# Performance work log

Measured on AMD Instinct MI355X. Metric: run time of the kernel, lower is better.

The kernel has to match this reference:

```python
import jax, jax.numpy as jnp
import numpy as np

B, S, D, H = 4, 2048, 1024, 16
DH = D // H


def setup_inputs() -> dict:
    key = jax.random.key(0)
    ks = jax.random.split(key, 6)
    scale = 1.0 / np.sqrt(D)  # xavier-ish scale for weights
    return {
        "x": jax.random.normal(ks[0], (B, S, D), dtype=jnp.float32),
        "M": jax.random.normal(ks[1], (B, D, D), dtype=jnp.float32) * scale,
        "mask": jnp.zeros((1, 1, S, S), dtype=jnp.float32),
        "Wq": jax.random.normal(ks[2], (D, D), dtype=jnp.float32) * scale,
        "Wk": jax.random.normal(ks[3], (D, D), dtype=jnp.float32) * scale,
        "Wv": jax.random.normal(ks[4], (D, D), dtype=jnp.float32) * scale,
        "Wo": jax.random.normal(ks[5], (D, D), dtype=jnp.float32) * scale,
    }


def reference(x, M, mask, Wq, Wk, Wv, Wo):
    # Projections (torch Linear: y = x @ W^T, bias=False)
    Q = jnp.einsum('bsd,ed->bse', x, Wq)
    K = jnp.einsum('bsd,ed->bse', x, Wk)
    V = jnp.einsum('bsd,ed->bse', x, Wv)
    # Archetypal metric: QM = Q @ M, per-batch bilinear transform on full d_model
    QM = jnp.einsum('bsd,bde->bse', Q, M)

    def split(t):  # [B,S,D] -> [B,H,S,DH]
        return t.reshape(B, S, H, DH).transpose(0, 2, 1, 3)

    QMh, Kh, Vh = split(QM), split(K), split(V)
    scores = jnp.einsum('bhsd,bhtd->bhst', QMh, Kh) / np.sqrt(DH)
    scores = jnp.clip(scores, -50.0, 50.0)
    scores = scores + mask  # broadcast additive mask
    attn = jax.nn.softmax(scores, axis=-1)  # dropout is identity (eval)
    out = jnp.einsum('bhst,bhtd->bhsd', attn, Vh)
    out = out.transpose(0, 2, 1, 3).reshape(B, S, D)  # merge heads
    return jnp.einsum('bsd,ed->bse', out, Wo)
```

## Files before the change

kernel.cpp:

```cpp
#include <hip/hip_runtime.h>
#include <cstdint>

typedef __attribute__((ext_vector_type(8))) short short8;
typedef __attribute__((ext_vector_type(8))) __bf16 bf16x8;
typedef __attribute__((ext_vector_type(4))) float f32x4;

__device__ __forceinline__ uint32_t cvt_pk_bf16(float lo, float hi) {
  uint32_t r;
  asm("v_cvt_pk_bf16_f32 %0, %1, %2" : "=v"(r) : "v"(lo), "v"(hi));
  return r;
}

__device__ __forceinline__ short f2bf(float f) {
  return (short)cvt_pk_bf16(f, f);
}

__device__ __forceinline__ float exp2_fast(float x) {
  return __builtin_amdgcn_exp2f(x);
}

__device__ __forceinline__ void mem_fence_compiler() {
  asm volatile("" ::: "memory");
}

__device__ __forceinline__ void gload_lds16(const void* g, void* l) {
  __builtin_amdgcn_global_load_lds(
      (const __attribute__((address_space(1))) void*)(uintptr_t)g,
      (__attribute__((address_space(3))) void*)(uint32_t)(uintptr_t)l,
      16, 0, 0);
}


__global__ __launch_bounds__(256) void cvt_f32_bf16(const float* __restrict__ s,
                                                    short* __restrict__ d, long n) {
  long i = ((long)blockIdx.x * 256 + threadIdx.x) * 8;
  if (i + 8 > n) return;
  const float4 a = *(const float4*)(s + i);
  const float4 b = *(const float4*)(s + i + 4);
  uint4 o;
  o.x = cvt_pk_bf16(a.x, a.y);
  o.y = cvt_pk_bf16(a.z, a.w);
  o.z = cvt_pk_bf16(b.x, b.y);
  o.w = cvt_pk_bf16(b.z, b.w);
  *(uint4*)(d + i) = o;
}

__global__ __launch_bounds__(256) void cvtT_M(const float* __restrict__ Msrc,
                                              short* __restrict__ Mt) {
  __shared__ short t[64][65];
  const int tid = threadIdx.x;
  const long bofs = (long)blockIdx.z * 1024 * 1024;
  const int d0 = blockIdx.x * 64, e0 = blockIdx.y * 64;
#pragma unroll
  for (int k = 0; k < 16; ++k) {
    int idx = k * 256 + tid; int r = idx >> 6, c = idx & 63;
    t[r][c] = f2bf(Msrc[bofs + (long)(d0 + r) * 1024 + e0 + c]);
  }
  __syncthreads();
#pragma unroll
  for (int k = 0; k < 16; ++k) {
    int idx = k * 256 + tid; int r = idx >> 6, c = idx & 63;
    Mt[bofs + (long)(e0 + r) * 1024 + d0 + c] = t[c][r];
  }
}

__global__ __launch_bounds__(256) void transposeV(const short* __restrict__ V,
                                                  short* __restrict__ Vt) {
  __shared__ short t[64][65];
  const int tid = threadIdx.x;
  const int s0 = blockIdx.x * 64, h = blockIdx.y;
  const long b = blockIdx.z;
  const short* src = V + (b * 2048) * 1024 + h * 64;
  short* dst = Vt + ((b * 16 + h) * 64) * 2048;
#pragma unroll
  for (int k = 0; k < 16; ++k) {
    int idx = k * 256 + tid; int r = idx >> 6, c = idx & 63;
    t[r][c] = src[(long)(s0 + r) * 1024 + c];
  }
  __syncthreads();
#pragma unroll
  for (int k = 0; k < 16; ++k) {
    int idx = k * 256 + tid; int r = idx >> 6, c = idx & 63;
    dst[(long)r * 2048 + s0 + c] = t[c][r];
  }
}

__global__ __launch_bounds__(256) void mask_flags(const float* __restrict__ mask,
                                                  int* __restrict__ flags) {
  __shared__ int f;
  const int tid = threadIdx.x;
  if (tid == 0) f = 0;
  __syncthreads();
  const int qt = blockIdx.x, tt = blockIdx.y;
  const float* base = mask + (long)qt * 64 * 2048 + tt * 64;
  const int r = tid >> 2, c = (tid & 3) * 16;
  bool nz = false;
#pragma unroll
  for (int k = 0; k < 4; ++k) {
    float4 v = *(const float4*)(base + (long)r * 2048 + c + k * 4);
    nz = nz | (v.x != 0.f) | (v.y != 0.f) | (v.z != 0.f) | (v.w != 0.f);
  }
  if (nz) f = 1;
  __syncthreads();
  if (tid == 0) flags[qt * 32 + tt] = f;
}


template <typename CT>
__global__ __launch_bounds__(256) void gemm_bt(
    const short* __restrict__ A, const short* __restrict__ B, CT* __restrict__ C,
    int M, int N, int K, long sA, long sB, long sC, float scale) {
  __shared__ __align__(16) short As[2][128 * 32];
  __shared__ __align__(16) short Bs[2][128 * 32];
  const int tid = threadIdx.x;
  const int w = tid >> 6, lane = tid & 63;
  const int wr = w >> 1, wc = w & 1;
  const int g = lane >> 4;
  const short* Ab = A + (long)blockIdx.z * sA + (long)blockIdx.x * 128 * K;
  const short* Bb = B + (long)blockIdx.z * sB + (long)blockIdx.y * 128 * K;

  f32x4 acc[4][4];
#pragma unroll
  for (int i = 0; i < 4; ++i)
#pragma unroll
    for (int j = 0; j < 4; ++j) acc[i][j] = {0.f, 0.f, 0.f, 0.f};

  const int srow = lane >> 2;
  const int scol = ((lane & 3) ^ (srow & 3)) * 8;

  auto STAGE = [&](int bufi, int k0) {
#pragma unroll
    for (int c = 0; c < 2; ++c) {
      const int chunk = w * 2 + c;
      const long gr = (long)(chunk * 16 + srow);
      gload_lds16(Ab + gr * K + k0 + scol, &As[bufi][chunk * 512]);
      gload_lds16(Bb + gr * K + k0 + scol, &Bs[bufi][chunk * 512]);
    }
  };

  auto COMPUTE = [&](int bufi) {
    bf16x8 af[4], bfr[4];
#pragma unroll
    for (int mf = 0; mf < 4; ++mf) {
      const int r = wr * 64 + mf * 16 + (lane & 15);
      const int cb = g ^ (r & 3);
      af[mf] = *(const bf16x8*)&As[bufi][r * 32 + cb * 8];
    }
#pragma unroll
    for (int nf = 0; nf < 4; ++nf) {
      const int r = wc * 64 + nf * 16 + (lane & 15);
      const int cb = g ^ (r & 3);
      bfr[nf] = *(const bf16x8*)&Bs[bufi][r * 32 + cb * 8];
    }
#pragma unroll
    for (int mf = 0; mf < 4; ++mf)
#pragma unroll
      for (int nf = 0; nf < 4; ++nf)
        acc[mf][nf] =
            __builtin_amdgcn_mfma_f32_16x16x32_bf16(af[mf], bfr[nf], acc[mf][nf], 0, 0, 0);
  };

  const int NK = K >> 5;
  STAGE(0, 0);
  for (int it = 0; it < NK; ++it) {
    const int cur = it & 1;
    if (it + 1 < NK) {
      STAGE(cur ^ 1, (it + 1) * 32);
      asm volatile("s_waitcnt vmcnt(4)" ::: "memory");
    } else {
      asm volatile("s_waitcnt vmcnt(0)" ::: "memory");
    }
    __builtin_amdgcn_s_barrier();
    __builtin_amdgcn_sched_barrier(0);
    COMPUTE(cur);
    __builtin_amdgcn_sched_barrier(0);
    __builtin_amdgcn_s_barrier();
  }

  CT* Cb = C + (long)blockIdx.z * sC;
  const int r0 = g * 4, cc = lane & 15;
#pragma unroll
  for (int mf = 0; mf < 4; ++mf)
#pragma unroll
    for (int i = 0; i < 4; ++i) {
      const long row = (long)blockIdx.x * 128 + wr * 64 + mf * 16 + r0 + i;
#pragma unroll
      for (int nf = 0; nf < 4; ++nf) {
        const long col = (long)blockIdx.y * 128 + wc * 64 + nf * 16 + cc;
        float v = acc[mf][nf][i] * scale;
        if constexpr (__is_same(CT, short))
          Cb[row * (long)N + col] = f2bf(v);
        else
          Cb[row * (long)N + col] = v;
      }
    }
}


__global__ __launch_bounds__(512) void flash_attn(
    const short* __restrict__ QM, const short* __restrict__ Kb,
    const short* __restrict__ Vt, const float* __restrict__ mask,
    const int* __restrict__ mflags, short* __restrict__ AO) {
  constexpr int S = 2048, D = 1024, NT = S / 64;
  constexpr float LOG2E = 1.44269504088896f;
  constexpr float CLIP = 50.0f * LOG2E;
  __shared__ __align__(16) short Ks[2][64 * 64];
  __shared__ __align__(16) short Vs[2][64 * 64];
  __shared__ __align__(16) short Ps[8][16 * 64];
  const int tid = threadIdx.x;
  const int w = tid >> 6, lane = tid & 63;
  const int q = lane & 15, g = lane >> 4;
  const int q0 = blockIdx.x * 128;
  const int h = blockIdx.y;
  const long b = blockIdx.z;

  const short* QMb = QM + (b * S) * D + h * 64;
  const short* Kbp = Kb + (b * S) * D + h * 64;
  const short* Vtp = Vt + ((b * 16 + h) * 64) * S;
  const int* flagrow = mflags + ((q0 + w * 16) >> 6) * 32;

  bf16x8 qf[2];
#pragma unroll
  for (int ks = 0; ks < 2; ++ks)
    qf[ks] = *(const bf16x8*)(QMb + (long)(q0 + w * 16 + q) * D + ks * 32 + g * 8);

  bf16x8 onesf;
#pragma unroll
  for (int j = 0; j < 8; ++j) onesf[j] = (__bf16)1.0f;

  f32x4 acc[4];
#pragma unroll
  for (int f = 0; f < 4; ++f) acc[f] = {0.f, 0.f, 0.f, 0.f};
  f32x4 acc_l = {0.f, 0.f, 0.f, 0.f};

  const int srow8 = lane >> 3;
  const int scol8 = ((lane & 7) ^ (srow8 & 7)) * 8;
  short* Pw = &Ps[w][0];
  const int psw = (q & 7) << 3;

  auto STAGE = [&](int bufi, int t0) {
    const int row = w * 8 + srow8;
    gload_lds16(Kbp + (long)(t0 + row) * D + scol8, &Ks[bufi][w * 512]);
    gload_lds16(Vtp + (long)row * S + t0 + scol8, &Vs[bufi][w * 512]);
  };

  auto COMPUTE = [&](int bufi, int t0) {
    f32x4 sacc[4];
#pragma unroll
    for (int nf = 0; nf < 4; ++nf) sacc[nf] = {0.f, 0.f, 0.f, 0.f};
    __builtin_amdgcn_s_setprio(1);
#pragma unroll
    for (int ks = 0; ks < 2; ++ks) {
#pragma unroll
      for (int nf = 0; nf < 4; ++nf) {
        const int r = nf * 16 + q;
        const int blk = (ks * 4 + g) ^ (r & 7);
        bf16x8 kf = *(const bf16x8*)&Ks[bufi][r * 64 + blk * 8];
        sacc[nf] = __builtin_amdgcn_mfma_f32_16x16x32_bf16(kf, qf[ks], sacc[nf], 0, 0, 0);
      }
    }
    __builtin_amdgcn_s_setprio(0);

    float pv[4][4];
    if (__builtin_expect(flagrow[t0 >> 6], 0)) {
      const float* mrow = mask + (long)(q0 + w * 16 + q) * S + t0;
#pragma unroll
      for (int nf = 0; nf < 4; ++nf) {
        float4 mv = *(const float4*)(mrow + nf * 16 + 4 * g);
        const float* mp = &mv.x;
#pragma unroll
        for (int i = 0; i < 4; ++i)
          pv[nf][i] = exp2_fast(
              __builtin_amdgcn_fmed3f(sacc[nf][i], -CLIP, CLIP) + LOG2E * mp[i]);
      }
    } else {
#pragma unroll
      for (int nf = 0; nf < 4; ++nf)
#pragma unroll
        for (int i = 0; i < 4; ++i)
          pv[nf][i] = exp2_fast(__builtin_amdgcn_fmed3f(sacc[nf][i], -CLIP, CLIP));
    }
#pragma unroll
    for (int nf = 0; nf < 4; ++nf) {
      uint2 u;
      u.x = cvt_pk_bf16(pv[nf][0], pv[nf][1]);
      u.y = cvt_pk_bf16(pv[nf][2], pv[nf][3]);
      *(uint2*)&Pw[q * 64 + ((nf * 16 + 4 * g) ^ psw)] = u;
    }

    mem_fence_compiler();

    __builtin_amdgcn_s_setprio(1);
#pragma unroll
    for (int ts = 0; ts < 2; ++ts) {
      bf16x8 pfr = *(const bf16x8*)&Pw[q * 64 + ((ts * 32 + 8 * g) ^ psw)];
#pragma unroll
      for (int f = 0; f < 4; ++f) {
        const int vr = f * 16 + q;
        const int vblk = (ts * 4 + g) ^ (vr & 7);
        bf16x8 vf = *(const bf16x8*)&Vs[bufi][vr * 64 + vblk * 8];
        acc[f] = __builtin_amdgcn_mfma_f32_16x16x32_bf16(vf, pfr, acc[f], 0, 0, 0);
      }
      acc_l = __builtin_amdgcn_mfma_f32_16x16x32_bf16(onesf, pfr, acc_l, 0, 0, 0);
    }
    __builtin_amdgcn_s_setprio(0);
    mem_fence_compiler();
  };

  STAGE(0, 0);
  for (int it = 0; it < NT; ++it) {
    const int cur = it & 1;
    if (it + 1 < NT) {
      STAGE(cur ^ 1, (it + 1) * 64);
      asm volatile("s_waitcnt vmcnt(2)" ::: "memory");
    } else {
      asm volatile("s_waitcnt vmcnt(0)" ::: "memory");
    }
    __builtin_amdgcn_s_barrier();
    __builtin_amdgcn_sched_barrier(0);
    COMPUTE(cur, it * 64);
    __builtin_amdgcn_sched_barrier(0);
    __builtin_amdgcn_s_barrier();
  }

  const float inv = 1.0f / acc_l[0];
#pragma unroll
  for (int f = 0; f < 4; ++f) {
    uint2 u;
    u.x = cvt_pk_bf16(acc[f][0] * inv, acc[f][1] * inv);
    u.y = cvt_pk_bf16(acc[f][2] * inv, acc[f][3] * inv);
    *(uint2*)&Pw[q * 64 + ((f * 16 + 4 * g) ^ psw)] = u;
  }
  mem_fence_compiler();
  const int qr = lane >> 2, c0 = (lane & 3) * 16;
  short* AOp = AO + (b * S) * D + h * 64;
#pragma unroll
  for (int r2 = 0; r2 < 2; ++r2) {
    const int cc2 = c0 + r2 * 8;
    bf16x8 ov = *(const bf16x8*)&Pw[qr * 64 + (cc2 ^ ((qr & 7) << 3))];
    *(bf16x8*)(AOp + (long)(q0 + w * 16 + qr) * D + cc2) = ov;
  }
}


extern "C" void kernel_launch(void* const* d_in, const int* in_sizes, int n_in,
                              void* d_out, int out_size, void* d_ws, size_t ws_size,
                              hipStream_t stream) {
  const float* x = (const float*)d_in[0];
  const float* M = (const float*)d_in[1];
  const float* mask = (const float*)d_in[2];
  const float* Wq = (const float*)d_in[3];
  const float* Wk = (const float*)d_in[4];
  const float* Wv = (const float*)d_in[5];
  const float* Wo = (const float*)d_in[6];
  float* out = (float*)d_out;

  constexpr long S = 2048, D = 1024;
  constexpr long NX = 4 * S * D;
  constexpr long NW = D * D;
  constexpr float C1 = 0.125f * 1.44269504088896f;

  short* p = (short*)d_ws;
  short* xb = p;   p += NX;
  short* wkb = p;  p += NW;
  short* wvb = p;  p += NW;
  short* wob = p;  p += NW;
  short* wqt = p;  p += NW;
  short* Mtb = p;  p += 4 * NW;
  short* Gtb = p;  p += 4 * NW;
  short* Kb = p;   p += NX;
  short* Vb = p;   p += NX;
  short* QMb = p;  p += NX;
  short* Vtb = p;  p += NX;
  int* flags = (int*)p;  p += 2048;
  short* AOb = Mtb;

  cvt_f32_bf16<<<NX / 2048, 256, 0, stream>>>(x, xb, NX);
  cvt_f32_bf16<<<NW / 2048, 256, 0, stream>>>(Wk, wkb, NW);
  cvt_f32_bf16<<<NW / 2048, 256, 0, stream>>>(Wv, wvb, NW);
  cvt_f32_bf16<<<NW / 2048, 256, 0, stream>>>(Wo, wob, NW);
  cvtT_M<<<dim3(16, 16, 1), 256, 0, stream>>>(Wq, wqt);
  cvtT_M<<<dim3(16, 16, 4), 256, 0, stream>>>(M, Mtb);
  mask_flags<<<dim3(32, 32), 256, 0, stream>>>(mask, flags);

  gemm_bt<short><<<dim3(64, 8, 2), 256, 0, stream>>>(xb, wkb, Kb, 8192, 1024, 1024,
                                                     0, NW, NX, 1.0f);
  gemm_bt<short><<<dim3(8, 8, 4), 256, 0, stream>>>(Mtb, wqt, Gtb, 1024, 1024, 1024,
                                                    NW, 0, NW, 1.0f);
  gemm_bt<short><<<dim3(16, 8, 4), 256, 0, stream>>>(xb, Gtb, QMb, 2048, 1024, 1024,
                                                     S * D, NW, S * D, C1);
  transposeV<<<dim3(32, 16, 4), 256, 0, stream>>>(Vb, Vtb);
  flash_attn<<<dim3(16, 16, 4), 512, 0, stream>>>(QMb, Kb, Vtb, mask, flags, AOb);
  gemm_bt<float><<<dim3(64, 8, 1), 256, 0, stream>>>(AOb, wob, out, 8192, 1024, 1024,
                                                     0, 0, 0, 1.0f);
}
```

Baseline: 248.7 us.

## Fuse V transpose into projection GEMM epilogue, triple-buffer GEMM, merge convert kernels

The K/V projection GEMM now writes V directly in transposed per-head layout through an LDS-staged epilogue, which removes the separate transposeV kernel and the intermediate V buffer. The GEMM main loop moves from double to triple buffering (prefetch two K-steps ahead), using more LDS per block. The weight conversion and transpose launches are merged into fewer kernels to cut launch overhead. The extra LDS could lower occupancy, and the transposed epilogue stores are 16-byte vectors spread across rows.

```diff
diff --git a/kernel.cpp b/kernel.cpp
--- a/kernel.cpp
+++ b/kernel.cpp
@@ -45,43 +45,44 @@
   *(uint4*)(d + i) = o;
 }
 
-__global__ __launch_bounds__(256) void cvtT_M(const float* __restrict__ Msrc,
-                                              short* __restrict__ Mt) {
+__global__ __launch_bounds__(256) void cvt3_f32_bf16(
+    const float* __restrict__ s0, short* __restrict__ d0,
+    const float* __restrict__ s1, short* __restrict__ d1,
+    const float* __restrict__ s2, short* __restrict__ d2) {
+  const int which = blockIdx.x >> 9;
+  const long i = (((long)(blockIdx.x & 511)) * 256 + threadIdx.x) * 8;
+  const float* s = which == 0 ? s0 : (which == 1 ? s1 : s2);
+  short* d = which == 0 ? d0 : (which == 1 ? d1 : d2);
+  const float4 a = *(const float4*)(s + i);
+  const float4 b = *(const float4*)(s + i + 4);
+  uint4 o;
+  o.x = cvt_pk_bf16(a.x, a.y);
+  o.y = cvt_pk_bf16(a.z, a.w);
+  o.z = cvt_pk_bf16(b.x, b.y);
+  o.w = cvt_pk_bf16(b.z, b.w);
+  *(uint4*)(d + i) = o;
+}
+
+__global__ __launch_bounds__(256) void cvtT5(const float* __restrict__ Wq,
+                                             short* __restrict__ wqt,
+                                             const float* __restrict__ M,
+                                             short* __restrict__ Mt) {
   __shared__ short t[64][65];
   const int tid = threadIdx.x;
-  const long bofs = (long)blockIdx.z * 1024 * 1024;
+  const int z = blockIdx.z;
+  const float* src = z == 0 ? Wq : M + (long)(z - 1) * 1024 * 1024;
+  short* dst = z == 0 ? wqt : Mt + (long)(z - 1) * 1024 * 1024;
   const int d0 = blockIdx.x * 64, e0 = blockIdx.y * 64;
 #pragma unroll
   for (int k = 0; k < 16; ++k) {
     int idx = k * 256 + tid; int r = idx >> 6, c = idx & 63;
-    t[r][c] = f2bf(Msrc[bofs + (long)(d0 + r) * 1024 + e0 + c]);
+    t[r][c] = f2bf(src[(long)(d0 + r) * 1024 + e0 + c]);
   }
   __syncthreads();
 #pragma unroll
   for (int k = 0; k < 16; ++k) {
     int idx = k * 256 + tid; int r = idx >> 6, c = idx & 63;
-    Mt[bofs + (long)(e0 + r) * 1024 + d0 + c] = t[c][r];
-  }
-}
-
-__global__ __launch_bounds__(256) void transposeV(const short* __restrict__ V,
-                                                  short* __restrict__ Vt) {
-  __shared__ short t[64][65];
-  const int tid = threadIdx.x;
-  const int s0 = blockIdx.x * 64, h = blockIdx.y;
-  const long b = blockIdx.z;
-  const short* src = V + (b * 2048) * 1024 + h * 64;
-  short* dst = Vt + ((b * 16 + h) * 64) * 2048;
-#pragma unroll
-  for (int k = 0; k < 16; ++k) {
-    int idx = k * 256 + tid; int r = idx >> 6, c = idx & 63;
-    t[r][c] = src[(long)(s0 + r) * 1024 + c];
-  }
-  __syncthreads();
-#pragma unroll
-  for (int k = 0; k < 16; ++k) {
-    int idx = k * 256 + tid; int r = idx >> 6, c = idx & 63;
-    dst[(long)r * 2048 + s0 + c] = t[c][r];
+    dst[(long)(e0 + r) * 1024 + d0 + c] = t[c][r];
   }
 }
 
@@ -109,9 +110,11 @@
 template <typename CT>
 __global__ __launch_bounds__(256) void gemm_bt(
     const short* __restrict__ A, const short* __restrict__ B, CT* __restrict__ C,
-    int M, int N, int K, long sA, long sB, long sC, float scale) {
-  __shared__ __align__(16) short As[2][128 * 32];
-  __shared__ __align__(16) short Bs[2][128 * 32];
+    int M, int N, int K, long sA, long sB, long sC, float scale,
+    short* __restrict__ vt) {
+  __shared__ __align__(16) short pool[24576];
+  short* Asb = pool;
+  short* Bsb = pool + 12288;
   const int tid = threadIdx.x;
   const int w = tid >> 6, lane = tid & 63;
   const int wr = w >> 1, wc = w & 1;
@@ -133,8 +136,8 @@
     for (int c = 0; c < 2; ++c) {
       const int chunk = w * 2 + c;
       const long gr = (long)(chunk * 16 + srow);
-      gload_lds16(Ab + gr * K + k0 + scol, &As[bufi][chunk * 512]);
-      gload_lds16(Bb + gr * K + k0 + scol, &Bs[bufi][chunk * 512]);
+      gload_lds16(Ab + gr * K + k0 + scol, Asb + bufi * 4096 + chunk * 512);
+      gload_lds16(Bb + gr * K + k0 + scol, Bsb + bufi * 4096 + chunk * 512);
     }
   };
 
@@ -144,13 +147,13 @@
     for (int mf = 0; mf < 4; ++mf) {
       const int r = wr * 64 + mf * 16 + (lane & 15);
       const int cb = g ^ (r & 3);
-      af[mf] = *(const bf16x8*)&As[bufi][r * 32 + cb * 8];
+      af[mf] = *(const bf16x8*)&Asb[bufi * 4096 + r * 32 + cb * 8];
     }
 #pragma unroll
     for (int nf = 0; nf < 4; ++nf) {
       const int r = wc * 64 + nf * 16 + (lane & 15);
       const int cb = g ^ (r & 3);
-      bfr[nf] = *(const bf16x8*)&Bs[bufi][r * 32 + cb * 8];
+      bfr[nf] = *(const bf16x8*)&Bsb[bufi * 4096 + r * 32 + cb * 8];
     }
 #pragma unroll
     for (int mf = 0; mf < 4; ++mf)
@@ -162,10 +165,13 @@
 
   const int NK = K >> 5;
   STAGE(0, 0);
+  if (NK > 1) STAGE(1, 32);
   for (int it = 0; it < NK; ++it) {
-    const int cur = it & 1;
-    if (it + 1 < NK) {
-      STAGE(cur ^ 1, (it + 1) * 32);
+    const int cur = it % 3;
+    if (it + 2 < NK) {
+      STAGE((it + 2) % 3, (it + 2) * 32);
+      asm volatile("s_waitcnt vmcnt(8)" ::: "memory");
+    } else if (it + 1 < NK) {
       asm volatile("s_waitcnt vmcnt(4)" ::: "memory");
     } else {
       asm volatile("s_waitcnt vmcnt(0)" ::: "memory");
@@ -177,8 +183,38 @@
     __builtin_amdgcn_s_barrier();
   }
 
+  const int r0 = g * 4, cc = lane & 15;
+  if (vt != nullptr && blockIdx.z == 1) {
+    __syncthreads();
+#pragma unroll
+    for (int mf = 0; mf < 4; ++mf)
+#pragma unroll
+      for (int i = 0; i < 4; ++i) {
+        const int srow_l = wr * 64 + mf * 16 + r0 + i;
+#pragma unroll
+        for (int nf = 0; nf < 4; ++nf) {
+          const int dh_l = wc * 64 + nf * 16 + cc;
+          pool[dh_l * 136 + srow_l] = f2bf(acc[mf][nf][i]);
+        }
+      }
+    __syncthreads();
+    const long bb = blockIdx.x >> 4;
+    const int s0b = (blockIdx.x & 15) * 128;
+    const int hbase = blockIdx.y * 2;
+#pragma unroll
+    for (int pass = 0; pass < 4; ++pass) {
+      const int dhrow = pass * 32 + (tid >> 3);
+      const long vrow = (bb * 16 + hbase + (dhrow >> 6)) * 64 + (dhrow & 63);
+      const int cseg = (tid & 7) * 16;
+      bf16x8 v0 = *(const bf16x8*)&pool[dhrow * 136 + cseg];
+      bf16x8 v1 = *(const bf16x8*)&pool[dhrow * 136 + cseg + 8];
+      *(bf16x8*)(vt + vrow * 2048 + s0b + cseg) = v0;
+      *(bf16x8*)(vt + vrow * 2048 + s0b + cseg + 8) = v1;
+    }
+    return;
+  }
+
   CT* Cb = C + (long)blockIdx.z * sC;
-  const int r0 = g * 4, cc = lane & 15;
 #pragma unroll
   for (int mf = 0; mf < 4; ++mf)
 #pragma unroll
@@ -369,28 +405,23 @@
   short* Mtb = p;  p += 4 * NW;
   short* Gtb = p;  p += 4 * NW;
   short* Kb = p;   p += NX;
-  short* Vb = p;   p += NX;
   short* QMb = p;  p += NX;
   short* Vtb = p;  p += NX;
   int* flags = (int*)p;  p += 2048;
   short* AOb = Mtb;
 
   cvt_f32_bf16<<<NX / 2048, 256, 0, stream>>>(x, xb, NX);
-  cvt_f32_bf16<<<NW / 2048, 256, 0, stream>>>(Wk, wkb, NW);
-  cvt_f32_bf16<<<NW / 2048, 256, 0, stream>>>(Wv, wvb, NW);
-  cvt_f32_bf16<<<NW / 2048, 256, 0, stream>>>(Wo, wob, NW);
-  cvtT_M<<<dim3(16, 16, 1), 256, 0, stream>>>(Wq, wqt);
-  cvtT_M<<<dim3(16, 16, 4), 256, 0, stream>>>(M, Mtb);
+  cvt3_f32_bf16<<<1536, 256, 0, stream>>>(Wk, wkb, Wv, wvb, Wo, wob);
+  cvtT5<<<dim3(16, 16, 5), 256, 0, stream>>>(Wq, wqt, M, Mtb);
   mask_flags<<<dim3(32, 32), 256, 0, stream>>>(mask, flags);
 
   gemm_bt<short><<<dim3(64, 8, 2), 256, 0, stream>>>(xb, wkb, Kb, 8192, 1024, 1024,
-                                                     0, NW, NX, 1.0f);
+                                                     0, NW, NX, 1.0f, Vtb);
   gemm_bt<short><<<dim3(8, 8, 4), 256, 0, stream>>>(Mtb, wqt, Gtb, 1024, 1024, 1024,
-                                                    NW, 0, NW, 1.0f);
+                                                    NW, 0, NW, 1.0f, nullptr);
   gemm_bt<short><<<dim3(16, 8, 4), 256, 0, stream>>>(xb, Gtb, QMb, 2048, 1024, 1024,
-                                                     S * D, NW, S * D, C1);
-  transposeV<<<dim3(32, 16, 4), 256, 0, stream>>>(Vb, Vtb);
+                                                     S * D, NW, S * D, C1, nullptr);
   flash_attn<<<dim3(16, 16, 4), 512, 0, stream>>>(QMb, Kb, Vtb, mask, flags, AOb);
   gemm_bt<float><<<dim3(64, 8, 1), 256, 0, stream>>>(AOb, wob, out, 8192, 1024, 1024,
-                                                     0, 0, 0, 1.0f);
-}
+                                                     0, 0, 0, 1.0f, nullptr);
+}
```

After: 236.1 us (median of 2 runs). -5.1%, faster.
